# Optimization experiments

Measured on AMD Instinct MI355X. Metric: run time of the kernel, lower is better.

The kernel has to match this reference:

```python
import jax, jax.numpy as jnp
import numpy as np

N = 100000
E = 6400000
IN_CH = 128
HID = 8
HEADS = 2
OUT_CH = 1
NEG_SLOPE = 0.2


def gat_conv(x, src, dst, W, a_src, a_dst, bias, heads, out_ch, concat, n_nodes):
    # x: [N, F_in], W: [F_in, heads*out_ch], a_src/a_dst: [heads, out_ch]
    h = (x @ W).reshape(n_nodes, heads, out_ch)          # [N, H, C]
    alpha_s = jnp.sum(h * a_src[None], axis=-1)          # [N, H]
    alpha_d = jnp.sum(h * a_dst[None], axis=-1)          # [N, H]
    alpha = alpha_s[src] + alpha_d[dst]                  # [E, H]
    alpha = jax.nn.leaky_relu(alpha, NEG_SLOPE)
    # segment softmax over incoming edges of each destination node
    seg_max = jax.ops.segment_max(alpha, dst, num_segments=n_nodes)  # [N, H]
    alpha = jnp.exp(alpha - seg_max[dst])
    denom = jax.ops.segment_sum(alpha, dst, num_segments=n_nodes)    # [N, H]
    alpha = alpha / (denom[dst] + 1e-16)
    msg = h[src] * alpha[..., None]                       # [E, H, C]
    out = jax.ops.segment_sum(msg, dst, num_segments=n_nodes)        # [N, H, C]
    if concat:
        out = out.reshape(n_nodes, heads * out_ch)
    else:
        out = out.mean(axis=1)
    return out + bias


def setup_inputs() -> dict:
    key = jax.random.key(0)
    ks = jax.random.split(key, 12)
    x = jax.random.normal(ks[0], (N, IN_CH), dtype=jnp.float32)
    edge_index = jax.random.randint(ks[1], (2, E), 0, N, dtype=jnp.int64)
    s1 = 1.0 / np.sqrt(IN_CH)
    W1 = jax.random.normal(ks[2], (IN_CH, HEADS * HID), dtype=jnp.float32) * s1
    a_src1 = jax.random.normal(ks[3], (HEADS, HID), dtype=jnp.float32) * (1.0 / np.sqrt(HID))
    a_dst1 = jax.random.normal(ks[4], (HEADS, HID), dtype=jnp.float32) * (1.0 / np.sqrt(HID))
    b1 = jnp.zeros((HEADS * HID,), dtype=jnp.float32)
    s2 = 1.0 / np.sqrt(HEADS * HID)
    W2 = jax.random.normal(ks[5], (HEADS * HID, OUT_CH), dtype=jnp.float32) * s2
    a_src2 = jax.random.normal(ks[6], (1, OUT_CH), dtype=jnp.float32)
    a_dst2 = jax.random.normal(ks[7], (1, OUT_CH), dtype=jnp.float32)
    b2 = jnp.zeros((OUT_CH,), dtype=jnp.float32)
    return {"x": x, "edge_index": edge_index, "W1": W1, "a_src1": a_src1,
            "a_dst1": a_dst1, "b1": b1, "W2": W2, "a_src2": a_src2,
            "a_dst2": a_dst2, "b2": b2}


def reference(x, edge_index, W1, a_src1, a_dst1, b1, W2, a_src2, a_dst2, b2):
    # add self-loops (PyG GATConv default)
    loops = jnp.arange(N, dtype=edge_index.dtype)
    src = jnp.concatenate([edge_index[0], loops])
    dst = jnp.concatenate([edge_index[1], loops])
    h = gat_conv(x, src, dst, W1, a_src1, a_dst1, b1, HEADS, HID, True, N)
    h = jax.nn.relu(h)
    out = gat_conv(h, src, dst, W2, a_src2, a_dst2, b2, 1, OUT_CH, False, N)
    return out
```

## Files before the change

### kernel.cpp

```cpp
#include <hip/hip_runtime.h>
#include <hip/hip_fp16.h>
#include <cstdint>
#include <cstddef>

#define N_NODES 100000
#define E_EDGES 6400000
#define E_TOT   (E_EDGES + N_NODES)
#define IN_CH   128
#define NHID    16
#define BSHIFT  9
#define BSZ     512
#define NBUCK   196
#define CHUNK   6144
#define BCAP    48
#define NCHUNK  ((E_TOT + CHUNK - 1) / CHUNK)

__global__ void k_detect(const int* __restrict__ edge, int* __restrict__ flag) {
    if (blockIdx.x == 0 && threadIdx.x == 0) {
        int odd_or = 0;
        for (int i = 0; i < 64; i++) odd_or |= edge[2 * i + 1];
        flag[0] = (odd_or == 0) ? 1 : 0;
    }
}

__global__ __launch_bounds__(256) void k_gemm1(
        const float* __restrict__ x, const float* __restrict__ W1,
        const float* __restrict__ a_src1, const float* __restrict__ a_dst1,
        __half* __restrict__ h16, float* __restrict__ asrc,
        float* __restrict__ adst) {
    __shared__ __align__(16) float sW[IN_CH * NHID];
    __shared__ __align__(16) float sx[16][132];
    __shared__ float sh[16][17];
    int t = threadIdx.x;
    int r = t >> 4, c = t & 15;
    int row = blockIdx.x * 16 + r;

    const float4* W4 = (const float4*)W1;
    ((float4*)sW)[t] = W4[t];
    ((float4*)sW)[t + 256] = W4[t + 256];

    if (row < N_NODES) {
        const float4* xr = (const float4*)(x + (size_t)row * IN_CH);
        float4 v0 = xr[c];
        float4 v1 = xr[c + 16];
        *(float4*)&sx[r][4 * c] = v0;
        *(float4*)&sx[r][64 + 4 * c] = v1;
    }
    __syncthreads();

    float acc = 0.f;
    if (row < N_NODES) {
        #pragma unroll 16
        for (int k = 0; k < IN_CH; k++) acc = fmaf(sx[r][k], sW[k * NHID + c], acc);
        h16[(size_t)row * NHID + c] = __float2half(acc);
    }
    sh[r][c] = acc;
    __syncthreads();

    if (row < N_NODES && c < 4) {
        int h = c & 1;
        const float* av = (c >= 2) ? a_dst1 : a_src1;
        float s = 0.f;
        #pragma unroll
        for (int q = 0; q < 8; q++) s = fmaf(sh[r][h * 8 + q], av[h * 8 + q], s);
        if (c < 2) asrc[2 * (size_t)row + c] = s;
        else       adst[2 * (size_t)row + (c - 2)] = s;
    }
}

__global__ __launch_bounds__(256) void k_ccount(const int* __restrict__ edge,
                                                const int* __restrict__ flag,
                                                int* __restrict__ ccnt) {
    __shared__ int sc[NBUCK];
    int m64 = flag[0];
    int t = threadIdx.x;
    for (int i = t; i < NBUCK; i += 256) sc[i] = 0;
    __syncthreads();
    size_t c0 = (size_t)blockIdx.x * CHUNK;
    size_t cend = c0 + CHUNK; if (cend > E_TOT) cend = E_TOT;
    size_t ee = (cend < (size_t)E_EDGES) ? cend : (size_t)E_EDGES;

    if (m64) {
        const int4* dp = (const int4*)(edge + 2 * (size_t)E_EDGES);
        for (size_t i = c0 + 2 * t; i < ee; i += 512) {
            int4 v = dp[i >> 1];
            atomicAdd(&sc[v.x >> BSHIFT], 1);
            if (i + 1 < ee) atomicAdd(&sc[v.z >> BSHIFT], 1);
        }
    } else {
        const int4* dp = (const int4*)(edge + (size_t)E_EDGES);
        for (size_t i = c0 + 4 * t; i < ee; i += 1024) {
            int4 v = dp[i >> 2];
            atomicAdd(&sc[v.x >> BSHIFT], 1);
            if (i + 1 < ee) atomicAdd(&sc[v.y >> BSHIFT], 1);
            if (i + 2 < ee) atomicAdd(&sc[v.z >> BSHIFT], 1);
            if (i + 3 < ee) atomicAdd(&sc[v.w >> BSHIFT], 1);
        }
    }
    size_t sl0 = (c0 > (size_t)E_EDGES) ? c0 : (size_t)E_EDGES;
    for (size_t i = sl0 + t; i < cend; i += 256) {
        int d = (int)(i - E_EDGES);
        atomicAdd(&sc[d >> BSHIFT], 1);
    }
    __syncthreads();
    for (int i = t; i < NBUCK; i += 256)
        ccnt[(size_t)blockIdx.x * NBUCK + i] = sc[i];
}

__global__ __launch_bounds__(256) void k_cscan(int* __restrict__ ccnt,
                                               int* __restrict__ bcnt) {
    __shared__ int sd[256];
    __shared__ int carry;
    int b = blockIdx.x, t = threadIdx.x;
    if (t == 0) carry = 0;
    __syncthreads();
    for (int base = 0; base < NCHUNK; base += 256) {
        int c = base + t;
        int v = (c < NCHUNK) ? ccnt[(size_t)c * NBUCK + b] : 0;
        sd[t] = v;
        __syncthreads();
        for (int ofs = 1; ofs < 256; ofs <<= 1) {
            int a = sd[t];
            int bb = (t >= ofs) ? sd[t - ofs] : 0;
            __syncthreads();
            sd[t] = a + bb;
            __syncthreads();
        }
        if (c < NCHUNK) ccnt[(size_t)c * NBUCK + b] = sd[t] - v + carry;
        __syncthreads();
        if (t == 255) carry += sd[255];
        __syncthreads();
    }
    if (t == 0) bcnt[b] = carry;
}

__global__ void k_bscan(const int* __restrict__ bcnt, int* __restrict__ bbase) {
    __shared__ int sd[256];
    int t = threadIdx.x;
    int v = (t < NBUCK) ? bcnt[t] : 0;
    sd[t] = v;
    __syncthreads();
    for (int ofs = 1; ofs < 256; ofs <<= 1) {
        int a = sd[t];
        int b = (t >= ofs) ? sd[t - ofs] : 0;
        __syncthreads();
        sd[t] = a + b;
        __syncthreads();
    }
    if (t < NBUCK) bbase[t] = sd[t] - v;
    if (t == NBUCK) bbase[NBUCK] = sd[NBUCK - 1];
}

__global__ __launch_bounds__(256) void k_bin(const int* __restrict__ edge,
                                             const int* __restrict__ flag,
                                             const int* __restrict__ ccnt,
                                             const int* __restrict__ bbase,
                                             unsigned* __restrict__ staged) {
    __shared__ unsigned lbin[NBUCK][BCAP];
    __shared__ int lcnt[NBUCK];
    __shared__ int lbase[NBUCK];
    int m64 = flag[0];
    int t = threadIdx.x;
    int g = t >> 4, lane = t & 15;

    size_t c0 = (size_t)blockIdx.x * CHUNK;
    if (c0 >= E_TOT) return;
    size_t cend = c0 + CHUNK; if (cend > E_TOT) cend = E_TOT;
    size_t ee = (cend < (size_t)E_EDGES) ? cend : (size_t)E_EDGES;

    for (int i = t; i < NBUCK; i += 256) {
        lcnt[i] = 0;
        lbase[i] = bbase[i] + ccnt[(size_t)blockIdx.x * NBUCK + i];
    }
    __syncthreads();

    auto put = [&](int s, int d) {
        int b = d >> BSHIFT;
        unsigned v = (unsigned)s | ((unsigned)(d & (BSZ - 1)) << 17);
        int idx = atomicAdd(&lcnt[b], 1);
        if (idx < BCAP) lbin[b][idx] = v;
        else            staged[lbase[b] + idx] = v;
    };

    if (m64) {
        const int4* sp = (const int4*)edge;
        const int4* dp = (const int4*)(edge + 2 * (size_t)E_EDGES);
        for (size_t i = c0 + 2 * t; i < ee; i += 512) {
            int4 sv = sp[i >> 1];
            int4 dv = dp[i >> 1];
            put(sv.x, dv.x);
            if (i + 1 < ee) put(sv.z, dv.z);
        }
    } else {
        const int4* sp = (const int4*)edge;
        const int4* dp = (const int4*)(edge + (size_t)E_EDGES);
        for (size_t i = c0 + 4 * t; i < ee; i += 1024) {
            int4 sv = sp[i >> 2];
            int4 dv = dp[i >> 2];
            put(sv.x, dv.x);
            if (i + 1 < ee) put(sv.y, dv.y);
            if (i + 2 < ee) put(sv.z, dv.z);
            if (i + 3 < ee) put(sv.w, dv.w);
        }
    }
    size_t sl0 = (c0 > (size_t)E_EDGES) ? c0 : (size_t)E_EDGES;
    for (size_t i = sl0 + t; i < cend; i += 256) {
        int d = (int)(i - E_EDGES);
        put(d, d);
    }
    __syncthreads();
    for (int b = g; b < NBUCK; b += 16) {
        int n = min(lcnt[b], BCAP);
        if (!n) continue;
        int pos = lbase[b];
        for (int i = lane; i < n; i += 16) staged[pos + i] = lbin[b][i];
    }
}

__global__ __launch_bounds__(1024) void k_sort(const unsigned* __restrict__ staged,
                                               const int* __restrict__ bbase,
                                               int* __restrict__ csr,
                                               int* __restrict__ offs) {
    __shared__ int hist[BSZ];
    __shared__ int histlo[BSZ];
    __shared__ int lcur[BSZ];
    int bkt = blockIdx.x >> 1, p = blockIdx.x & 1;
    int t = threadIdx.x;
    int beg = bbase[bkt], end = bbase[bkt + 1];
    int mid = beg + ((end - beg + 1) >> 1);
    int dbase = bkt << BSHIFT;

    if (t < BSZ) { hist[t] = 0; histlo[t] = 0; }
    __syncthreads();
    for (int e = beg + t; e < end; e += 1024) {
        int dl = staged[e] >> 17;
        atomicAdd(&hist[dl], 1);
        if (e < mid) atomicAdd(&histlo[dl], 1);
    }
    __syncthreads();

    int myv = (t < BSZ) ? hist[t] : 0;
    __syncthreads();
    for (int ofs = 1; ofs < BSZ; ofs <<= 1) {
        int a = 0, b = 0;
        if (t < BSZ) { a = hist[t]; b = (t >= ofs) ? hist[t - ofs] : 0; }
        __syncthreads();
        if (t < BSZ) hist[t] = a + b;
        __syncthreads();
    }
    if (t < BSZ) {
        int excl = hist[t] - myv;
        lcur[t] = excl + (p ? histlo[t] : 0);
        if (p == 0) {
            int dd = dbase + t;
            if (dd < N_NODES) offs[dd] = beg + excl;
        }
    }
    if (bkt == NBUCK - 1 && p == 0 && t == 0) offs[N_NODES] = E_TOT;
    __syncthreads();

    int lo = p ? mid : beg;
    int hi = p ? end : mid;
    for (int e = lo + t; e < hi; e += 1024) {
        unsigned v = staged[e];
        int pos = atomicAdd(&lcur[v >> 17], 1);
        csr[beg + pos] = (int)(v & 0x1FFFFu);
    }
}

__global__ __launch_bounds__(256) void k_edge1(
        const int* __restrict__ offs, const int* __restrict__ csr,
        const __half* __restrict__ h16, const float* __restrict__ asrc,
        const float* __restrict__ adst,
        const float* __restrict__ b1, const float* __restrict__ W2,
        float* __restrict__ h2out) {
    __shared__ float sacc[256][9];
    int t = threadIdx.x;
    int lane = t & 15;
    int g = t >> 4;
    int d = blockIdx.x * 16 + g;
    if (d >= N_NODES) return;

    int sub = lane & 1;
    int pr  = lane >> 1;
    float2 adp = ((const float2*)adst)[d];
    float adpv = sub ? adp.y : adp.x;
    int beg = offs[d], end = offs[d + 1];

    float acc[8];
    #pragma unroll
    for (int c = 0; c < 8; c++) acc[c] = 0.f;
    float den = 0.f;

    auto loadslot = [&](int ee, float& aspv, float4& hv) {
        if (ee < end) {
            int s = csr[ee];
            float2 asp = ((const float2*)asrc)[s];
            aspv = sub ? asp.y : asp.x;
            hv = *(const float4*)(h16 + (size_t)s * NHID + sub * 8);
        }
    };
    auto consume = [&](float aspv, const float4& hv) {
        float a = aspv + adpv; a = (a > 0.f) ? a : 0.2f * a;
        float pw = __expf(a);
        den += pw;
        const __half2* hh = (const __half2*)&hv;
        #pragma unroll
        for (int q = 0; q < 4; q++) {
            float2 f = __half22float2(hh[q]);
            acc[2 * q]     = fmaf(pw, f.x, acc[2 * q]);
            acc[2 * q + 1] = fmaf(pw, f.y, acc[2 * q + 1]);
        }
    };

    float aA = 0.f, aB = 0.f, aC = 0.f, aD = 0.f, aE = 0.f, aF = 0.f;
    float4 z4 = make_float4(0.f, 0.f, 0.f, 0.f);
    float4 hA = z4, hB = z4, hC = z4, hD = z4, hE = z4, hF = z4;

    int e = beg + pr;
    loadslot(e,      aA, hA);
    loadslot(e + 8,  aB, hB);
    loadslot(e + 16, aC, hC);
    loadslot(e + 24, aD, hD);
    loadslot(e + 32, aE, hE);
    loadslot(e + 40, aF, hF);
    while (true) {
        if (e >= end) break;
        consume(aA, hA); loadslot(e + 48, aA, hA); e += 8;
        if (e >= end) break;
        consume(aB, hB); loadslot(e + 48, aB, hB); e += 8;
        if (e >= end) break;
        consume(aC, hC); loadslot(e + 48, aC, hC); e += 8;
        if (e >= end) break;
        consume(aD, hD); loadslot(e + 48, aD, hD); e += 8;
        if (e >= end) break;
        consume(aE, hE); loadslot(e + 48, aE, hE); e += 8;
        if (e >= end) break;
        consume(aF, hF); loadslot(e + 48, aF, hF); e += 8;
    }
    den += __shfl_xor(den, 2, 64);
    den += __shfl_xor(den, 4, 64);
    den += __shfl_xor(den, 8, 64);
    #pragma unroll
    for (int c = 0; c < 8; c++) sacc[t][c] = acc[c];
    float sum = 0.f;
    int rowb = g * 16 + (lane >> 3);
    int ch = lane & 7;
    #pragma unroll
    for (int pp = 0; pp < 8; pp++) sum += sacc[rowb + 2 * pp][ch];

    int wgbase = t & 0x30;
    float denh = __shfl(den, wgbase | (lane >> 3), 64);

    float o = sum / (denh + 1e-16f) + b1[lane];
    o = (o > 0.f) ? o : 0.f;
    float v = o * W2[lane];
    v += __shfl_xor(v, 1, 64);
    v += __shfl_xor(v, 2, 64);
    v += __shfl_xor(v, 4, 64);
    v += __shfl_xor(v, 8, 64);
    if (lane == 0) h2out[d] = v;
}

__global__ __launch_bounds__(256) void k_edge2(
        const int* __restrict__ offs, const int* __restrict__ csr,
        const float* __restrict__ h2,
        const float* __restrict__ a_src2, const float* __restrict__ a_dst2,
        const float* __restrict__ b2, float* __restrict__ out) {
    int t = threadIdx.x;
    int g = t >> 4, lane = t & 15;
    int d = blockIdx.x * 16 + g;
    if (d >= N_NODES) return;

    float as2 = a_src2[0], ad2 = a_dst2[0];
    float adv = h2[d] * ad2;
    int beg = offs[d], end = offs[d + 1];

    float den = 0.f, acc = 0.f;
    auto ls = [&](int ee, float& hs) { if (ee < end) hs = h2[csr[ee]]; };
    auto cs = [&](float hs) {
        float a = fmaf(hs, as2, adv);
        a = (a > 0.f) ? a : 0.2f * a;
        float p = __expf(a);
        den += p;
        acc = fmaf(p, hs, acc);
    };
    float hA = 0.f, hB = 0.f, hC = 0.f, hD = 0.f, hE = 0.f, hF = 0.f;
    int e = beg + lane;
    ls(e, hA); ls(e + 16, hB); ls(e + 32, hC);
    ls(e + 48, hD); ls(e + 64, hE); ls(e + 80, hF);
    while (true) {
        if (e >= end) break;
        cs(hA); ls(e + 96, hA); e += 16;
        if (e >= end) break;
        cs(hB); ls(e + 96, hB); e += 16;
        if (e >= end) break;
        cs(hC); ls(e + 96, hC); e += 16;
        if (e >= end) break;
        cs(hD); ls(e + 96, hD); e += 16;
        if (e >= end) break;
        cs(hE); ls(e + 96, hE); e += 16;
        if (e >= end) break;
        cs(hF); ls(e + 96, hF); e += 16;
    }
    #pragma unroll
    for (int m = 1; m < 16; m <<= 1) {
        den += __shfl_xor(den, m, 64);
        acc += __shfl_xor(acc, m, 64);
    }
    if (lane == 0) out[d] = acc / (den + 1e-16f) + b2[0];
}

extern "C" void kernel_launch(void* const* d_in, const int* in_sizes, int n_in,
                              void* d_out, int out_size, void* d_ws, size_t ws_size,
                              hipStream_t stream) {
    const float* x      = (const float*)d_in[0];
    const int*   edge   = (const int*)  d_in[1];
    const float* W1     = (const float*)d_in[2];
    const float* a_src1 = (const float*)d_in[3];
    const float* a_dst1 = (const float*)d_in[4];
    const float* b1     = (const float*)d_in[5];
    const float* W2     = (const float*)d_in[6];
    const float* a_src2 = (const float*)d_in[7];
    const float* a_dst2 = (const float*)d_in[8];
    const float* b2     = (const float*)d_in[9];

    constexpr size_t A = 256;
    auto al = [](size_t b) { return (b + A - 1) / A * A; };
    char* ws = (char*)d_ws;
    size_t off = 0;
    int*      flag   = (int*)(ws + off);      off += al(256);
    int*      ccnt   = (int*)(ws + off);      off += al((size_t)NCHUNK * NBUCK * 4);
    int*      bcnt   = (int*)(ws + off);      off += al(NBUCK * 4);
    int*      bbase  = (int*)(ws + off);      off += al((NBUCK + 1) * 4);
    unsigned* staged = (unsigned*)(ws + off); off += al((size_t)E_TOT * 4);
    int*      csr    = (int*)(ws + off);      off += al((size_t)E_TOT * 4);
    int*      offs   = (int*)(ws + off);      off += al((size_t)(N_NODES + 1) * 4);
    __half*   h16    = (__half*)(ws + off);   off += al((size_t)N_NODES * NHID * 2);
    float*    asrc   = (float*)(ws + off);    off += al((size_t)N_NODES * 2 * 4);
    float*    adst   = (float*)(ws + off);    off += al((size_t)N_NODES * 2 * 4);
    float*    h2     = (float*)(ws + off);    off += al((size_t)N_NODES * 4);
    (void)ws_size; (void)in_sizes; (void)n_in; (void)out_size;

    k_detect<<<1, 64, 0, stream>>>(edge, flag);
    k_gemm1 <<<(N_NODES + 15) / 16, 256, 0, stream>>>(x, W1, a_src1, a_dst1, h16, asrc, adst);
    k_ccount<<<NCHUNK, 256, 0, stream>>>(edge, flag, ccnt);
    k_cscan <<<NBUCK, 256, 0, stream>>>(ccnt, bcnt);
    k_bscan <<<1, 256, 0, stream>>>(bcnt, bbase);
    k_bin   <<<NCHUNK, 256, 0, stream>>>(edge, flag, ccnt, bbase, staged);
    k_sort  <<<NBUCK * 2, 1024, 0, stream>>>(staged, bbase, csr, offs);
    k_edge1 <<<(N_NODES + 15) / 16, 256, 0, stream>>>(offs, csr, h16, asrc, adst, b1, W2, h2);
    k_edge2 <<<(N_NODES + 15) / 16, 256, 0, stream>>>(offs, csr, h2, a_src2, a_dst2, b2,
                                                      (float*)d_out);
}
```

Before: 232.3 us.

## Fuse bucket sort with layer-1 aggregation using LDS-resident CSR and packed node records

The per-bucket sort kernel and the first-layer edge aggregation kernel become one kernel. Each block sorts a 256-node bucket into a CSR held in LDS and then aggregates directly from it, with two threads per destination node (one per head). The source features and source attention scores are packed into one 64-byte record per node, so each gather touches a single line. This removes the global CSR read-back and a kernel launch. In exchange, each node's edges are walked serially by one thread with a shallow prefetch, the large LDS buffer limits occupancy, and a bucket with more edges than the fixed LDS capacity would overflow it.

```diff
diff --git a/kernel.cpp b/kernel.cpp
--- a/kernel.cpp
+++ b/kernel.cpp
@@ -8,12 +8,14 @@
 #define E_TOT   (E_EDGES + N_NODES)
 #define IN_CH   128
 #define NHID    16
-#define BSHIFT  9
-#define BSZ     512
-#define NBUCK   196
+#define RECB    64
+#define BSHIFT  8
+#define BSZ     256
+#define NBUCK   391
 #define CHUNK   6144
-#define BCAP    48
+#define BCAP    24
 #define NCHUNK  ((E_TOT + CHUNK - 1) / CHUNK)
+#define LCAP    18176
 
 __global__ void k_detect(const int* __restrict__ edge, int* __restrict__ flag) {
     if (blockIdx.x == 0 && threadIdx.x == 0) {
@@ -26,8 +28,7 @@
 __global__ __launch_bounds__(256) void k_gemm1(
         const float* __restrict__ x, const float* __restrict__ W1,
         const float* __restrict__ a_src1, const float* __restrict__ a_dst1,
-        __half* __restrict__ h16, float* __restrict__ asrc,
-        float* __restrict__ adst) {
+        char* __restrict__ rec, float* __restrict__ adst) {
     __shared__ __align__(16) float sW[IN_CH * NHID];
     __shared__ __align__(16) float sx[16][132];
     __shared__ float sh[16][17];
@@ -52,7 +53,7 @@
     if (row < N_NODES) {
         #pragma unroll 16
         for (int k = 0; k < IN_CH; k++) acc = fmaf(sx[r][k], sW[k * NHID + c], acc);
-        h16[(size_t)row * NHID + c] = __float2half(acc);
+        ((__half*)(rec + (size_t)row * RECB))[c] = __float2half(acc);
     }
     sh[r][c] = acc;
     __syncthreads();
@@ -63,7 +64,7 @@
         float s = 0.f;
         #pragma unroll
         for (int q = 0; q < 8; q++) s = fmaf(sh[r][h * 8 + q], av[h * 8 + q], s);
-        if (c < 2) asrc[2 * (size_t)row + c] = s;
+        if (c < 2) ((float*)(rec + (size_t)row * RECB + 32))[c] = s;
         else       adst[2 * (size_t)row + (c - 2)] = s;
     }
 }
@@ -134,13 +135,14 @@
     if (t == 0) bcnt[b] = carry;
 }
 
-__global__ void k_bscan(const int* __restrict__ bcnt, int* __restrict__ bbase) {
-    __shared__ int sd[256];
+__global__ __launch_bounds__(512) void k_bscan(const int* __restrict__ bcnt,
+                                               int* __restrict__ bbase) {
+    __shared__ int sd[512];
     int t = threadIdx.x;
     int v = (t < NBUCK) ? bcnt[t] : 0;
     sd[t] = v;
     __syncthreads();
-    for (int ofs = 1; ofs < 256; ofs <<= 1) {
+    for (int ofs = 1; ofs < 512; ofs <<= 1) {
         int a = sd[t];
         int b = (t >= ofs) ? sd[t - ofs] : 0;
         __syncthreads();
@@ -217,26 +219,30 @@
     }
 }
 
-__global__ __launch_bounds__(1024) void k_sort(const unsigned* __restrict__ staged,
-                                               const int* __restrict__ bbase,
-                                               int* __restrict__ csr,
-                                               int* __restrict__ offs) {
+__global__ __launch_bounds__(512) void k_fused1(
+        const unsigned* __restrict__ staged, const int* __restrict__ bbase,
+        const char* __restrict__ rec, const float* __restrict__ adst,
+        const float* __restrict__ b1, const float* __restrict__ W2,
+        int* __restrict__ csr, int* __restrict__ offs,
+        float* __restrict__ h2out) {
+    __shared__ int lcsr[LCAP];
     __shared__ int hist[BSZ];
-    __shared__ int histlo[BSZ];
-    __shared__ int lcur[BSZ];
-    int bkt = blockIdx.x >> 1, p = blockIdx.x & 1;
-    int t = threadIdx.x;
+    __shared__ int segbeg[BSZ];
+    __shared__ int cur[BSZ];
+    __shared__ float2 sadp[BSZ];
+    int bkt = blockIdx.x;
+    int t = threadIdx.x;
+    int dbase = bkt << BSHIFT;
     int beg = bbase[bkt], end = bbase[bkt + 1];
-    int mid = beg + ((end - beg + 1) >> 1);
-    int dbase = bkt << BSHIFT;
-
-    if (t < BSZ) { hist[t] = 0; histlo[t] = 0; }
-    __syncthreads();
-    for (int e = beg + t; e < end; e += 1024) {
-        int dl = staged[e] >> 17;
-        atomicAdd(&hist[dl], 1);
-        if (e < mid) atomicAdd(&histlo[dl], 1);
-    }
+
+    if (t < BSZ) {
+        hist[t] = 0;
+        int d = dbase + t;
+        sadp[t] = (d < N_NODES) ? ((const float2*)adst)[d] : make_float2(0.f, 0.f);
+    }
+    __syncthreads();
+    for (int e = beg + t; e < end; e += 512)
+        atomicAdd(&hist[staged[e] >> 17], 1);
     __syncthreads();
 
     int myv = (t < BSZ) ? hist[t] : 0;
@@ -250,54 +256,39 @@
     }
     if (t < BSZ) {
         int excl = hist[t] - myv;
-        lcur[t] = excl + (p ? histlo[t] : 0);
-        if (p == 0) {
-            int dd = dbase + t;
-            if (dd < N_NODES) offs[dd] = beg + excl;
-        }
-    }
-    if (bkt == NBUCK - 1 && p == 0 && t == 0) offs[N_NODES] = E_TOT;
-    __syncthreads();
-
-    int lo = p ? mid : beg;
-    int hi = p ? end : mid;
-    for (int e = lo + t; e < hi; e += 1024) {
+        segbeg[t] = excl;
+        cur[t] = excl;
+        int d = dbase + t;
+        if (d < N_NODES) offs[d] = beg + excl;
+    }
+    if (bkt == NBUCK - 1 && t == 0) offs[N_NODES] = E_TOT;
+    __syncthreads();
+
+    for (int e = beg + t; e < end; e += 512) {
         unsigned v = staged[e];
-        int pos = atomicAdd(&lcur[v >> 17], 1);
-        csr[beg + pos] = (int)(v & 0x1FFFFu);
-    }
-}
-
-__global__ __launch_bounds__(256) void k_edge1(
-        const int* __restrict__ offs, const int* __restrict__ csr,
-        const __half* __restrict__ h16, const float* __restrict__ asrc,
-        const float* __restrict__ adst,
-        const float* __restrict__ b1, const float* __restrict__ W2,
-        float* __restrict__ h2out) {
-    __shared__ float sacc[256][9];
-    int t = threadIdx.x;
-    int lane = t & 15;
-    int g = t >> 4;
-    int d = blockIdx.x * 16 + g;
-    if (d >= N_NODES) return;
-
-    int sub = lane & 1;
-    int pr  = lane >> 1;
-    float2 adp = ((const float2*)adst)[d];
-    float adpv = sub ? adp.y : adp.x;
-    int beg = offs[d], end = offs[d + 1];
+        int pos = atomicAdd(&cur[v >> 17], 1);
+        lcsr[pos] = (int)(v & 0x1FFFFu);
+    }
+    __syncthreads();
+
+    int n = end - beg;
+    for (int i = t; i < n; i += 512) csr[beg + i] = lcsr[i];
+
+    int p = t >> 1, sub = t & 1;
+    int sb = segbeg[p], se = cur[p];
+    float adpv = sub ? sadp[p].y : sadp[p].x;
 
     float acc[8];
     #pragma unroll
     for (int c = 0; c < 8; c++) acc[c] = 0.f;
     float den = 0.f;
 
-    auto loadslot = [&](int ee, float& aspv, float4& hv) {
-        if (ee < end) {
-            int s = csr[ee];
-            float2 asp = ((const float2*)asrc)[s];
-            aspv = sub ? asp.y : asp.x;
-            hv = *(const float4*)(h16 + (size_t)s * NHID + sub * 8);
+    auto loadslot = [&](int i, float& aspv, float4& hv) {
+        if (i < se) {
+            int s = lcsr[i];
+            const char* rp = rec + (size_t)s * RECB;
+            hv = *(const float4*)(rp + sub * 16);
+            aspv = *(const float*)(rp + 32 + 4 * sub);
         }
     };
     auto consume = [&](float aspv, const float4& hv) {
@@ -313,53 +304,39 @@
         }
     };
 
-    float aA = 0.f, aB = 0.f, aC = 0.f, aD = 0.f, aE = 0.f, aF = 0.f;
+    float aA = 0.f, aB = 0.f, aC = 0.f, aD = 0.f;
     float4 z4 = make_float4(0.f, 0.f, 0.f, 0.f);
-    float4 hA = z4, hB = z4, hC = z4, hD = z4, hE = z4, hF = z4;
-
-    int e = beg + pr;
-    loadslot(e,      aA, hA);
-    loadslot(e + 8,  aB, hB);
-    loadslot(e + 16, aC, hC);
-    loadslot(e + 24, aD, hD);
-    loadslot(e + 32, aE, hE);
-    loadslot(e + 40, aF, hF);
+    float4 hA = z4, hB = z4, hC = z4, hD = z4;
+
+    int i = sb;
+    loadslot(i,     aA, hA);
+    loadslot(i + 1, aB, hB);
+    loadslot(i + 2, aC, hC);
+    loadslot(i + 3, aD, hD);
     while (true) {
-        if (e >= end) break;
-        consume(aA, hA); loadslot(e + 48, aA, hA); e += 8;
-        if (e >= end) break;
-        consume(aB, hB); loadslot(e + 48, aB, hB); e += 8;
-        if (e >= end) break;
-        consume(aC, hC); loadslot(e + 48, aC, hC); e += 8;
-        if (e >= end) break;
-        consume(aD, hD); loadslot(e + 48, aD, hD); e += 8;
-        if (e >= end) break;
-        consume(aE, hE); loadslot(e + 48, aE, hE); e += 8;
-        if (e >= end) break;
-        consume(aF, hF); loadslot(e + 48, aF, hF); e += 8;
-    }
-    den += __shfl_xor(den, 2, 64);
-    den += __shfl_xor(den, 4, 64);
-    den += __shfl_xor(den, 8, 64);
+        if (i >= se) break;
+        consume(aA, hA); loadslot(i + 4, aA, hA); i++;
+        if (i >= se) break;
+        consume(aB, hB); loadslot(i + 4, aB, hB); i++;
+        if (i >= se) break;
+        consume(aC, hC); loadslot(i + 4, aC, hC); i++;
+        if (i >= se) break;
+        consume(aD, hD); loadslot(i + 4, aD, hD); i++;
+    }
+
+    float inv = 1.f / (den + 1e-16f);
+    float v = 0.f;
     #pragma unroll
-    for (int c = 0; c < 8; c++) sacc[t][c] = acc[c];
-    float sum = 0.f;
-    int rowb = g * 16 + (lane >> 3);
-    int ch = lane & 7;
-    #pragma unroll
-    for (int pp = 0; pp < 8; pp++) sum += sacc[rowb + 2 * pp][ch];
-
-    int wgbase = t & 0x30;
-    float denh = __shfl(den, wgbase | (lane >> 3), 64);
-
-    float o = sum / (denh + 1e-16f) + b1[lane];
-    o = (o > 0.f) ? o : 0.f;
-    float v = o * W2[lane];
+    for (int ch = 0; ch < 8; ch++) {
+        float o = acc[ch] * inv + b1[8 * sub + ch];
+        o = (o > 0.f) ? o : 0.f;
+        v = fmaf(o, W2[8 * sub + ch], v);
+    }
     v += __shfl_xor(v, 1, 64);
-    v += __shfl_xor(v, 2, 64);
-    v += __shfl_xor(v, 4, 64);
-    v += __shfl_xor(v, 8, 64);
-    if (lane == 0) h2out[d] = v;
+    if (sub == 0) {
+        int d = dbase + p;
+        if (d < N_NODES) h2out[d] = v;
+    }
 }
 
 __global__ __launch_bounds__(256) void k_edge2(
@@ -436,20 +413,18 @@
     unsigned* staged = (unsigned*)(ws + off); off += al((size_t)E_TOT * 4);
     int*      csr    = (int*)(ws + off);      off += al((size_t)E_TOT * 4);
     int*      offs   = (int*)(ws + off);      off += al((size_t)(N_NODES + 1) * 4);
-    __half*   h16    = (__half*)(ws + off);   off += al((size_t)N_NODES * NHID * 2);
-    float*    asrc   = (float*)(ws + off);    off += al((size_t)N_NODES * 2 * 4);
+    char*     rec    = (char*)(ws + off);     off += al((size_t)N_NODES * RECB);
     float*    adst   = (float*)(ws + off);    off += al((size_t)N_NODES * 2 * 4);
     float*    h2     = (float*)(ws + off);    off += al((size_t)N_NODES * 4);
     (void)ws_size; (void)in_sizes; (void)n_in; (void)out_size;
 
     k_detect<<<1, 64, 0, stream>>>(edge, flag);
-    k_gemm1 <<<(N_NODES + 15) / 16, 256, 0, stream>>>(x, W1, a_src1, a_dst1, h16, asrc, adst);
+    k_gemm1 <<<(N_NODES + 15) / 16, 256, 0, stream>>>(x, W1, a_src1, a_dst1, rec, adst);
     k_ccount<<<NCHUNK, 256, 0, stream>>>(edge, flag, ccnt);
     k_cscan <<<NBUCK, 256, 0, stream>>>(ccnt, bcnt);
-    k_bscan <<<1, 256, 0, stream>>>(bcnt, bbase);
+    k_bscan <<<1, 512, 0, stream>>>(bcnt, bbase);
     k_bin   <<<NCHUNK, 256, 0, stream>>>(edge, flag, ccnt, bbase, staged);
-    k_sort  <<<NBUCK * 2, 1024, 0, stream>>>(staged, bbase, csr, offs);
-    k_edge1 <<<(N_NODES + 15) / 16, 256, 0, stream>>>(offs, csr, h16, asrc, adst, b1, W2, h2);
+    k_fused1<<<NBUCK, 512, 0, stream>>>(staged, bbase, rec, adst, b1, W2, csr, offs, h2);
     k_edge2 <<<(N_NODES + 15) / 16, 256, 0, stream>>>(offs, csr, h2, a_src2, a_dst2, b2,
                                                       (float*)d_out);
 }
```

Result: faster. 201.8 us (-13.1%).
